# Kernel tuning notes

Hardware: AMD Instinct MI355X
Metric: run time of the kernel (lower is better)

The kernel has to match this reference:

```python
import jax, jax.numpy as jnp
import numpy as np


def _conv3x3(x, w, stride=1):
    # x: [N, C_in, H, W], w: [C_out, C_in, 3, 3] (ternary {-1,0,1}), padding=1, no bias
    return jax.lax.conv_general_dilated(
        x, w,
        window_strides=(stride, stride),
        padding=((1, 1), (1, 1)),
        dimension_numbers=("NCHW", "OIHW", "NCHW"),
    )


def _bn(x, gamma, beta, mean, var, eps=1e-5):
    # inference-mode BatchNorm2d over channel dim
    inv = gamma * jax.lax.rsqrt(var + eps)
    return x * inv[None, :, None, None] + (beta - mean * inv)[None, :, None, None]


def setup_inputs() -> dict:
    key = jax.random.key(0)
    ks = jax.random.split(key, 8)
    N, C, H, W = 64, 256, 32, 32
    x = jax.random.normal(ks[0], (N, C, H, W), dtype=jnp.float32)
    # Ternary conv weights in {-1, 0, +1} (scale_and_shift=False => raw ternary values)
    w1 = jax.random.randint(ks[1], (C, C, 3, 3), -1, 2).astype(jnp.float32)
    w2 = jax.random.randint(ks[2], (C, C, 3, 3), -1, 2).astype(jnp.float32)
    # BatchNorm affine params and running stats
    g1 = jax.random.normal(ks[3], (C,), dtype=jnp.float32) * 0.1 + 1.0
    b1 = jax.random.normal(ks[4], (C,), dtype=jnp.float32) * 0.1
    g2 = jax.random.normal(ks[5], (C,), dtype=jnp.float32) * 0.1 + 1.0
    b2 = jax.random.normal(ks[6], (C,), dtype=jnp.float32) * 0.1
    rm1 = jnp.zeros((C,), dtype=jnp.float32)
    rv1 = jnp.ones((C,), dtype=jnp.float32)
    rm2 = jnp.zeros((C,), dtype=jnp.float32)
    rv2 = jnp.ones((C,), dtype=jnp.float32)
    return {"x": x, "w1": w1, "g1": g1, "b1": b1, "rm1": rm1, "rv1": rv1,
            "w2": w2, "g2": g2, "b2": b2, "rm2": rm2, "rv2": rv2}


def reference(x, w1, g1, b1, rm1, rv1, w2, g2, b2, rm2, rv2):
    # BasicBlock forward: stride=1, downsample=None -> identity skip
    h = _conv3x3(x, w1, stride=1)
    h = _bn(h, g1, b1, rm1, rv1)
    h = jax.nn.relu(h)
    h = _conv3x3(h, w2, stride=1)
    h = _bn(h, g2, b2, rm2, rv2)
    return jax.nn.relu(x + h)
```

## Files before the change

kernel.cpp:

```cpp
#include <hip/hip_runtime.h>

typedef unsigned short u16;
typedef unsigned int u32;
typedef __attribute__((ext_vector_type(8))) short bf16x8;
typedef __attribute__((ext_vector_type(4))) float f32x4;

__device__ __forceinline__ u16 f2bf(float f) {
    u32 u = __float_as_uint(f);
    u += 0x7fffu + ((u >> 16) & 1u);
    return (u16)(u >> 16);
}

__device__ __forceinline__ void llds16(void* l, const void* g) {
    __builtin_amdgcn_global_load_lds(
        (const __attribute__((address_space(1))) u32*)g,
        (__attribute__((address_space(3))) u32*)l, 16, 0, 0);
}

__global__ void prep_scale(const float* __restrict__ g1, const float* __restrict__ b1,
                           const float* __restrict__ rm1, const float* __restrict__ rv1,
                           const float* __restrict__ g2, const float* __restrict__ b2,
                           const float* __restrict__ rm2, const float* __restrict__ rv2,
                           float* __restrict__ sc, float* __restrict__ zp) {
    int t = threadIdx.x;
    float s1 = g1[t] * rsqrtf(rv1[t] + 1e-5f);
    sc[t]       = s1;
    sc[256 + t] = b1[t] - rm1[t] * s1;
    float s2 = g2[t] * rsqrtf(rv2[t] + 1e-5f);
    sc[512 + t] = s2;
    sc[768 + t] = b2[t] - rm2[t] * s2;
    zp[t] = 0.0f;
}

__global__ void prep_x(const float* __restrict__ x, u16* __restrict__ xt) {
    __shared__ float xl[32 * 33];
    int b = blockIdx.x;
    int n = b >> 8, rem = b & 255;
    int h = rem >> 3, c0 = (rem & 7) << 5;
    int t = threadIdx.x;
    int cl = t >> 5, w = t & 31;
#pragma unroll
    for (int i = 0; i < 4; ++i) {
        int c = c0 + i * 8 + cl;
        xl[(i * 8 + cl) * 33 + w] = x[(n * 256 + c) * 1024 + h * 32 + w];
    }
    __syncthreads();
    int wo = t >> 3, k = t & 7;
    ushort4 o;
    o.x = f2bf(xl[(k * 4 + 0) * 33 + wo]);
    o.y = f2bf(xl[(k * 4 + 1) * 33 + wo]);
    o.z = f2bf(xl[(k * 4 + 2) * 33 + wo]);
    o.w = f2bf(xl[(k * 4 + 3) * 33 + wo]);
    *(ushort4*)&xt[((n * 32 + h) * 32 + wo) * 256 + c0 + k * 4] = o;
}

__global__ void prep_w(const float* __restrict__ w1, const float* __restrict__ w2,
                       u16* __restrict__ W1t, u16* __restrict__ W2t) {
    int idx = blockIdx.x * 256 + threadIdx.x;
    const float* src = blockIdx.y ? w2 : w1;
    u16* dst = blockIdx.y ? W2t : W1t;
    const float* s = src + idx * 9;
    int co = idx >> 8, ci = idx & 255;
#pragma unroll
    for (int p = 0; p < 9; ++p)
        dst[p * 65536 + co * 256 + ci] = f2bf(s[p]);
}

__global__ __launch_bounds__(256, 2) void conv_mfma(
    const u16* __restrict__ Xt,
    const u16* __restrict__ Wt,
    const float* __restrict__ sv,
    const float* __restrict__ tv,
    const float* __restrict__ skip,
    u16* __restrict__ ybf,
    float* __restrict__ yf,
    const u16* __restrict__ zp, int stage)
{
    __shared__ alignas(16) u16 ldsA[9 * 64 * 32];
    __shared__ alignas(16) u16 ldsB[10 * 34 * 32];

    int t = threadIdx.x;
    int wv = t >> 6, lane = t & 63;
    int q = lane >> 4, n16 = lane & 15, q8 = q * 8;
    int co0 = blockIdx.x << 6, h0 = blockIdx.y << 3, nb = blockIdx.z;
    int hbase = wv << 1;

    if (t < 160) {
        int hh = t >> 4, side = (t >> 3) & 1, o8 = t & 7;
        ushort4 z; z.x = 0; z.y = 0; z.z = 0; z.w = 0;
        *(ushort4*)&ldsB[hh * 1088 + side * 1056 + o8 * 4] = z;
    }

    f32x4 acc[4][4] = {};

    for (int kc = 0; kc < 256; kc += 32) {
#pragma unroll
        for (int i = 0; i < 9; ++i) {
            int g = wv * 9 + i;
            int p = g >> 2, co = ((g & 3) << 4) + (lane >> 2), ci = (lane & 3) << 3;
            const u16* gp = Wt + (p << 16) + ((co0 + co) << 8) + kc + ci;
            llds16(&ldsA[g << 9], gp);
        }
#pragma unroll
        for (int j = 0; j < 5; ++j) {
            int g = wv * 5 + j;
            int hh = g >> 1, half = g & 1;
            int w = (half << 4) + (lane >> 2), ci = (lane & 3) << 3;
            int hin = h0 - 1 + hh;
            const u16* gp = (hin >= 0 && hin < 32)
                          ? (Xt + ((nb * 32 + hin) * 32 + w) * 256 + kc + ci)
                          : (zp + lane * 8);
            llds16(&ldsB[hh * 1088 + 32 + (half << 9)], gp);
        }
        asm volatile("s_waitcnt vmcnt(0)" ::: "memory");
        __syncthreads();

#pragma unroll
        for (int p = 0; p < 9; ++p) {
            const int kh = p / 3, kw = p % 3;
            bf16x8 aF[4], bF[4];
#pragma unroll
            for (int mt = 0; mt < 4; ++mt)
                aF[mt] = *(const bf16x8*)&ldsA[(p << 11) + (((mt << 4) + n16) << 5) + q8];
#pragma unroll
            for (int nt = 0; nt < 4; ++nt) {
                int hi = hbase + (nt >> 1) + kh;
                int wp = ((nt & 1) << 4) + n16 + kw;
                bF[nt] = *(const bf16x8*)&ldsB[hi * 1088 + wp * 32 + q8];
            }
#pragma unroll
            for (int mt = 0; mt < 4; ++mt)
#pragma unroll
                for (int nt = 0; nt < 4; ++nt)
                    acc[mt][nt] = __builtin_amdgcn_mfma_f32_16x16x32_bf16(
                        aF[mt], bF[nt], acc[mt][nt], 0, 0, 0);
        }
        __syncthreads();
    }

    if (stage == 1) {
#pragma unroll
        for (int mt = 0; mt < 4; ++mt) {
            int cb = co0 + (mt << 4) + (q << 2);
            f32x4 ss = *(const f32x4*)&sv[cb];
            f32x4 tt = *(const f32x4*)&tv[cb];
#pragma unroll
            for (int nt = 0; nt < 4; ++nt) {
                int h = h0 + hbase + (nt >> 1), w = ((nt & 1) << 4) + n16;
                ushort4 o;
                o.x = f2bf(fmaxf(acc[mt][nt][0] * ss[0] + tt[0], 0.f));
                o.y = f2bf(fmaxf(acc[mt][nt][1] * ss[1] + tt[1], 0.f));
                o.z = f2bf(fmaxf(acc[mt][nt][2] * ss[2] + tt[2], 0.f));
                o.w = f2bf(fmaxf(acc[mt][nt][3] * ss[3] + tt[3], 0.f));
                *(ushort4*)&ybf[(((nb << 5) + h) * 32 + w) * 256 + cb] = o;
            }
        }
    } else {
#pragma unroll
        for (int mt = 0; mt < 4; ++mt) {
            int cb = co0 + (mt << 4) + (q << 2);
            f32x4 ss = *(const f32x4*)&sv[cb];
            f32x4 tt = *(const f32x4*)&tv[cb];
#pragma unroll
            for (int nt = 0; nt < 4; ++nt) {
                int h = h0 + hbase + (nt >> 1), w = ((nt & 1) << 4) + n16;
#pragma unroll
                for (int j = 0; j < 4; ++j) {
                    int idx = (((nb << 8) + cb + j) << 10) + (h << 5) + w;
                    yf[idx] = fmaxf(acc[mt][nt][j] * ss[j] + tt[j] + skip[idx], 0.f);
                }
            }
        }
    }
}

extern "C" void kernel_launch(void* const* d_in, const int* in_sizes, int n_in,
                              void* d_out, int out_size, void* d_ws, size_t ws_size,
                              hipStream_t stream) {
    const float* x   = (const float*)d_in[0];
    const float* w1  = (const float*)d_in[1];
    const float* g1  = (const float*)d_in[2];
    const float* b1  = (const float*)d_in[3];
    const float* rm1 = (const float*)d_in[4];
    const float* rv1 = (const float*)d_in[5];
    const float* w2  = (const float*)d_in[6];
    const float* g2  = (const float*)d_in[7];
    const float* b2  = (const float*)d_in[8];
    const float* rm2 = (const float*)d_in[9];
    const float* rv2 = (const float*)d_in[10];

    char* ws = (char*)d_ws;
    u16*  XT  = (u16*)(ws);
    u16*  H1  = (u16*)(ws + 33554432);
    u16*  W1t = (u16*)(ws + 67108864);
    u16*  W2t = (u16*)(ws + 68288512);
    float* sc = (float*)(ws + 69468160);
    u16*  zpg = (u16*)(ws + 69472256);
    if (ws_size < 69473280) return;

    prep_scale<<<1, 256, 0, stream>>>(g1, b1, rm1, rv1, g2, b2, rm2, rv2, sc, (float*)zpg);
    prep_x<<<16384, 256, 0, stream>>>(x, XT);
    prep_w<<<dim3(256, 2), 256, 0, stream>>>(w1, w2, W1t, W2t);

    dim3 grid(4, 4, 64);
    conv_mfma<<<grid, 256, 0, stream>>>(XT, W1t, sc, sc + 256, nullptr,
                                        H1, nullptr, zpg, 1);
    conv_mfma<<<grid, 256, 0, stream>>>(H1, W2t, sc + 512, sc + 768, x,
                                        nullptr, (float*)d_out, zpg, 2);
}
```

Baseline: 273.9 us.

## Fuse prep kernels and restructure conv LDS layout for fragment-order loads

Merges the three preprocessing kernels into a single launch, which removes launch overhead. In the conv kernel, the LDS tiles are rearranged so that each lane's global_load_lds destination matches MFMA fragment order, including the zero padding columns, so the separate padding-zeroing step is no longer needed. Global source pointers are precomputed once outside the K loop. The inner loop is reordered to load B fragments once per kw and reuse them across the three kh taps, which cuts LDS reads. The trade-off is higher register pressure from the cached pointers and fragments, plus the new layout may bring different LDS bank-conflict patterns.

```diff
diff --git a/kernel.cpp b/kernel.cpp
--- a/kernel.cpp
+++ b/kernel.cpp
@@ -17,53 +17,55 @@
         (__attribute__((address_space(3))) u32*)l, 16, 0, 0);
 }
 
-__global__ void prep_scale(const float* __restrict__ g1, const float* __restrict__ b1,
-                           const float* __restrict__ rm1, const float* __restrict__ rv1,
-                           const float* __restrict__ g2, const float* __restrict__ b2,
-                           const float* __restrict__ rm2, const float* __restrict__ rv2,
-                           float* __restrict__ sc, float* __restrict__ zp) {
+__global__ void prep(const float* __restrict__ x, u16* __restrict__ xt,
+                     const float* __restrict__ w1, const float* __restrict__ w2,
+                     u16* __restrict__ W1t, u16* __restrict__ W2t,
+                     const float* __restrict__ g1, const float* __restrict__ b1,
+                     const float* __restrict__ rm1, const float* __restrict__ rv1,
+                     const float* __restrict__ g2, const float* __restrict__ b2,
+                     const float* __restrict__ rm2, const float* __restrict__ rv2,
+                     float* __restrict__ sc, u32* __restrict__ zp) {
     int t = threadIdx.x;
-    float s1 = g1[t] * rsqrtf(rv1[t] + 1e-5f);
-    sc[t]       = s1;
-    sc[256 + t] = b1[t] - rm1[t] * s1;
-    float s2 = g2[t] * rsqrtf(rv2[t] + 1e-5f);
-    sc[512 + t] = s2;
-    sc[768 + t] = b2[t] - rm2[t] * s2;
-    zp[t] = 0.0f;
-}
-
-__global__ void prep_x(const float* __restrict__ x, u16* __restrict__ xt) {
-    __shared__ float xl[32 * 33];
     int b = blockIdx.x;
-    int n = b >> 8, rem = b & 255;
-    int h = rem >> 3, c0 = (rem & 7) << 5;
-    int t = threadIdx.x;
-    int cl = t >> 5, w = t & 31;
-#pragma unroll
-    for (int i = 0; i < 4; ++i) {
-        int c = c0 + i * 8 + cl;
-        xl[(i * 8 + cl) * 33 + w] = x[(n * 256 + c) * 1024 + h * 32 + w];
-    }
-    __syncthreads();
-    int wo = t >> 3, k = t & 7;
-    ushort4 o;
-    o.x = f2bf(xl[(k * 4 + 0) * 33 + wo]);
-    o.y = f2bf(xl[(k * 4 + 1) * 33 + wo]);
-    o.z = f2bf(xl[(k * 4 + 2) * 33 + wo]);
-    o.w = f2bf(xl[(k * 4 + 3) * 33 + wo]);
-    *(ushort4*)&xt[((n * 32 + h) * 32 + wo) * 256 + c0 + k * 4] = o;
-}
-
-__global__ void prep_w(const float* __restrict__ w1, const float* __restrict__ w2,
-                       u16* __restrict__ W1t, u16* __restrict__ W2t) {
-    int idx = blockIdx.x * 256 + threadIdx.x;
-    const float* src = blockIdx.y ? w2 : w1;
-    u16* dst = blockIdx.y ? W2t : W1t;
-    const float* s = src + idx * 9;
-    int co = idx >> 8, ci = idx & 255;
-#pragma unroll
-    for (int p = 0; p < 9; ++p)
-        dst[p * 65536 + co * 256 + ci] = f2bf(s[p]);
+    if (b < 16384) {
+        __shared__ float xl[32 * 33];
+        int n = b >> 8, rem = b & 255;
+        int h = rem >> 3, c0 = (rem & 7) << 5;
+        int cl = t >> 5, w = t & 31;
+#pragma unroll
+        for (int i = 0; i < 4; ++i) {
+            int c = c0 + i * 8 + cl;
+            xl[(i * 8 + cl) * 33 + w] = x[(n * 256 + c) * 1024 + h * 32 + w];
+        }
+        __syncthreads();
+        int wo = t >> 3, k = t & 7;
+        ushort4 o;
+        o.x = f2bf(xl[(k * 4 + 0) * 33 + wo]);
+        o.y = f2bf(xl[(k * 4 + 1) * 33 + wo]);
+        o.z = f2bf(xl[(k * 4 + 2) * 33 + wo]);
+        o.w = f2bf(xl[(k * 4 + 3) * 33 + wo]);
+        *(ushort4*)&xt[((n * 32 + h) * 32 + wo) * 256 + c0 + k * 4] = o;
+    } else {
+        int bb = b - 16384;
+        int idx = (bb & 255) * 256 + t;
+        const float* src = (bb >> 8) ? w2 : w1;
+        u16* dst = (bb >> 8) ? W2t : W1t;
+        const float* s = src + idx * 9;
+        int co = idx >> 8, ci = idx & 255;
+#pragma unroll
+        for (int p = 0; p < 9; ++p)
+            dst[p * 65536 + co * 256 + ci] = f2bf(s[p]);
+        if (bb == 0) {
+            float s1 = g1[t] * rsqrtf(rv1[t] + 1e-5f);
+            sc[t]       = s1;
+            sc[256 + t] = b1[t] - rm1[t] * s1;
+            float s2 = g2[t] * rsqrtf(rv2[t] + 1e-5f);
+            sc[512 + t] = s2;
+            sc[768 + t] = b2[t] - rm2[t] * s2;
+            zp[t] = 0u;
+            zp[t + 256] = 0u;
+        }
+    }
 }
 
 __global__ __launch_bounds__(256, 2) void conv_mfma(
@@ -76,64 +78,78 @@
     float* __restrict__ yf,
     const u16* __restrict__ zp, int stage)
 {
-    __shared__ alignas(16) u16 ldsA[9 * 64 * 32];
-    __shared__ alignas(16) u16 ldsB[10 * 34 * 32];
+    __shared__ alignas(16) u16 ldsA[9 * 4 * 64 * 8];
+    __shared__ alignas(16) u16 ldsB[22 * 64 * 8];
 
     int t = threadIdx.x;
     int wv = t >> 6, lane = t & 63;
-    int q = lane >> 4, n16 = lane & 15, q8 = q * 8;
+    int q = lane >> 4, n16 = lane & 15;
     int co0 = blockIdx.x << 6, h0 = blockIdx.y << 3, nb = blockIdx.z;
-    int hbase = wv << 1;
-
-    if (t < 160) {
-        int hh = t >> 4, side = (t >> 3) & 1, o8 = t & 7;
-        ushort4 z; z.x = 0; z.y = 0; z.z = 0; z.w = 0;
-        *(ushort4*)&ldsB[hh * 1088 + side * 1056 + o8 * 4] = z;
+
+    const u16* aSrc[9];
+#pragma unroll
+    for (int i = 0; i < 9; ++i) {
+        int g = wv * 9 + i;
+        int p = g >> 2, mt = g & 3;
+        aSrc[i] = Wt + (p << 16) + ((co0 + (mt << 4) + n16) << 8) + (q << 3);
+    }
+    const u16* bSrc[6];
+#pragma unroll
+    for (int j = 0; j < 6; ++j) {
+        int g2 = wv * 6 + j;
+        if (g2 < 22) {
+            int s = g2 * 64 + lane;
+            int hi = s / 136, rem = s - hi * 136;
+            int wp = rem >> 2, qq = rem & 3;
+            int hin = h0 - 1 + hi;
+            bool v = (wp >= 1) && (wp <= 32) && (hin >= 0) && (hin < 32);
+            bSrc[j] = v ? (Xt + (((nb << 5) + hin) * 32 + (wp - 1)) * 256 + (qq << 3))
+                        : (zp + lane * 8);
+        } else {
+            bSrc[j] = zp + lane * 8;
+        }
     }
 
     f32x4 acc[4][4] = {};
 
     for (int kc = 0; kc < 256; kc += 32) {
 #pragma unroll
-        for (int i = 0; i < 9; ++i) {
-            int g = wv * 9 + i;
-            int p = g >> 2, co = ((g & 3) << 4) + (lane >> 2), ci = (lane & 3) << 3;
-            const u16* gp = Wt + (p << 16) + ((co0 + co) << 8) + kc + ci;
-            llds16(&ldsA[g << 9], gp);
-        }
-#pragma unroll
-        for (int j = 0; j < 5; ++j) {
-            int g = wv * 5 + j;
-            int hh = g >> 1, half = g & 1;
-            int w = (half << 4) + (lane >> 2), ci = (lane & 3) << 3;
-            int hin = h0 - 1 + hh;
-            const u16* gp = (hin >= 0 && hin < 32)
-                          ? (Xt + ((nb * 32 + hin) * 32 + w) * 256 + kc + ci)
-                          : (zp + lane * 8);
-            llds16(&ldsB[hh * 1088 + 32 + (half << 9)], gp);
+        for (int i = 0; i < 9; ++i)
+            llds16(&ldsA[(wv * 9 + i) << 9], aSrc[i] + kc);
+#pragma unroll
+        for (int j = 0; j < 6; ++j) {
+            int g2 = wv * 6 + j;
+            if (g2 < 22) llds16(&ldsB[g2 << 9], bSrc[j] + kc);
         }
         asm volatile("s_waitcnt vmcnt(0)" ::: "memory");
         __syncthreads();
 
 #pragma unroll
-        for (int p = 0; p < 9; ++p) {
-            const int kh = p / 3, kw = p % 3;
-            bf16x8 aF[4], bF[4];
-#pragma unroll
-            for (int mt = 0; mt < 4; ++mt)
-                aF[mt] = *(const bf16x8*)&ldsA[(p << 11) + (((mt << 4) + n16) << 5) + q8];
-#pragma unroll
-            for (int nt = 0; nt < 4; ++nt) {
-                int hi = hbase + (nt >> 1) + kh;
-                int wp = ((nt & 1) << 4) + n16 + kw;
-                bF[nt] = *(const bf16x8*)&ldsB[hi * 1088 + wp * 32 + q8];
+        for (int kw = 0; kw < 3; ++kw) {
+            bf16x8 bFr[4][2];
+#pragma unroll
+            for (int r = 0; r < 4; ++r)
+#pragma unroll
+                for (int half = 0; half < 2; ++half) {
+                    int hi = (wv << 1) + r;
+                    int wp = (half << 4) + n16 + kw;
+                    bFr[r][half] = *(const bf16x8*)
+                        &ldsB[(hi * 136 + (wp << 2) + q) << 3];
+                }
+#pragma unroll
+            for (int kh = 0; kh < 3; ++kh) {
+                int p = kh * 3 + kw;
+                bf16x8 aF[4];
+#pragma unroll
+                for (int mt = 0; mt < 4; ++mt)
+                    aF[mt] = *(const bf16x8*)&ldsA[((p << 8) + (mt << 6) + lane) << 3];
+#pragma unroll
+                for (int mt = 0; mt < 4; ++mt)
+#pragma unroll
+                    for (int nt = 0; nt < 4; ++nt)
+                        acc[mt][nt] = __builtin_amdgcn_mfma_f32_16x16x32_bf16(
+                            aF[mt], bFr[(nt >> 1) + kh][nt & 1], acc[mt][nt], 0, 0, 0);
             }
-#pragma unroll
-            for (int mt = 0; mt < 4; ++mt)
-#pragma unroll
-                for (int nt = 0; nt < 4; ++nt)
-                    acc[mt][nt] = __builtin_amdgcn_mfma_f32_16x16x32_bf16(
-                        aF[mt], bF[nt], acc[mt][nt], 0, 0, 0);
         }
         __syncthreads();
     }
@@ -146,7 +162,7 @@
             f32x4 tt = *(const f32x4*)&tv[cb];
 #pragma unroll
             for (int nt = 0; nt < 4; ++nt) {
-                int h = h0 + hbase + (nt >> 1), w = ((nt & 1) << 4) + n16;
+                int h = h0 + (wv << 1) + (nt >> 1), w = ((nt & 1) << 4) + n16;
                 ushort4 o;
                 o.x = f2bf(fmaxf(acc[mt][nt][0] * ss[0] + tt[0], 0.f));
                 o.y = f2bf(fmaxf(acc[mt][nt][1] * ss[1] + tt[1], 0.f));
@@ -163,7 +179,7 @@
             f32x4 tt = *(const f32x4*)&tv[cb];
 #pragma unroll
             for (int nt = 0; nt < 4; ++nt) {
-                int h = h0 + hbase + (nt >> 1), w = ((nt & 1) << 4) + n16;
+                int h = h0 + (wv << 1) + (nt >> 1), w = ((nt & 1) << 4) + n16;
 #pragma unroll
                 for (int j = 0; j < 4; ++j) {
                     int idx = (((nb << 8) + cb + j) << 10) + (h << 5) + w;
@@ -195,16 +211,16 @@
     u16*  W1t = (u16*)(ws + 67108864);
     u16*  W2t = (u16*)(ws + 68288512);
     float* sc = (float*)(ws + 69468160);
-    u16*  zpg = (u16*)(ws + 69472256);
-    if (ws_size < 69473280) return;
-
-    prep_scale<<<1, 256, 0, stream>>>(g1, b1, rm1, rv1, g2, b2, rm2, rv2, sc, (float*)zpg);
-    prep_x<<<16384, 256, 0, stream>>>(x, XT);
-    prep_w<<<dim3(256, 2), 256, 0, stream>>>(w1, w2, W1t, W2t);
+    u32*  zpg = (u32*)(ws + 69472256);
+    if (ws_size < 69474304) return;
+
+    prep<<<16896, 256, 0, stream>>>(x, XT, w1, w2, W1t, W2t,
+                                    g1, b1, rm1, rv1, g2, b2, rm2, rv2,
+                                    sc, zpg);
 
     dim3 grid(4, 4, 64);
     conv_mfma<<<grid, 256, 0, stream>>>(XT, W1t, sc, sc + 256, nullptr,
-                                        H1, nullptr, zpg, 1);
+                                        H1, nullptr, (const u16*)zpg, 1);
     conv_mfma<<<grid, 256, 0, stream>>>(H1, W2t, sc + 512, sc + 768, x,
-                                        nullptr, (float*)d_out, zpg, 2);
-}
+                                        nullptr, (float*)d_out, (const u16*)zpg, 2);
+}
```

Measured after the change: 274.6 us. Within noise of the previous version (+0.3%).
